# Kernel tuning notes

Hardware: AMD Instinct MI355X
Metric: run time of the kernel (lower is better)

Reference implementation:

```python
import jax, jax.numpy as jnp
import numpy as np

B, T, C = 16, 512, 768
MULT = 4
D_IN = C * MULT          # 3072
HIDDEN = 1024
N_DATES = 16
STACK_SIZE, STACK_STRIDE = 4, 2
MAX_F = 512
N_MASK_TYPES = 5
N_SESSIONS = 4
SCALE = HIDDEN ** 0.5


def setup_inputs() -> dict:
    key = jax.random.key(0)
    ks = jax.random.split(key, 12)
    inp = {
        "spikes": jax.random.normal(ks[0], (B, T, C), dtype=jnp.float32),
        "spikes_mask": jnp.ones((B, T), dtype=jnp.int64),
        "spikes_timestamp": jax.random.randint(ks[1], (B, T), 0, 255).astype(jnp.int64),
        "date_idx": jax.random.randint(ks[2], (B,), 0, N_DATES).astype(jnp.int64),
        "mask_idx": 1,
        "session_idx": 3,
        # params
        "W_embed": jax.random.normal(ks[3], (N_DATES, D_IN, C), dtype=jnp.float32) * 0.02,
        "b_embed": jax.random.normal(ks[4], (N_DATES, D_IN), dtype=jnp.float32) * 0.02,
        "W_stack": jax.random.normal(ks[5], (HIDDEN, D_IN * STACK_SIZE), dtype=jnp.float32) * 0.02,
        "b_stack": jax.random.normal(ks[6], (HIDDEN,), dtype=jnp.float32) * 0.02,
        "pos_table": jax.random.normal(ks[7], (MAX_F, HIDDEN), dtype=jnp.float32) * 0.02,
        "prompt_table": jax.random.normal(ks[8], (N_MASK_TYPES, HIDDEN), dtype=jnp.float32) * 0.02,
        "session_table": jax.random.normal(ks[9], (N_SESSIONS, HIDDEN), dtype=jnp.float32) * 0.02,
    }
    return inp


def reference(spikes, spikes_mask, spikes_timestamp, date_idx, mask_idx, session_idx,
              W_embed, b_embed, W_stack, b_stack, pos_table, prompt_table, session_table):
    Bb = spikes.shape[0]
    # adapt branch: per-sample expert Linear, done as one gather + batched GEMM
    W = W_embed[date_idx]                      # [B, D_IN, C]
    b = b_embed[date_idx]                      # [B, D_IN]
    x = jnp.einsum('btc,bdc->btd', spikes, W) + b[:, None, :]   # [B, T, D_IN]
    x = jax.nn.gelu(x, approximate=False) * SCALE
    # unfold-based stacking: sliding windows over time
    L = (T - STACK_SIZE) // STACK_STRIDE + 1   # 255
    starts = jnp.arange(L) * STACK_STRIDE
    widx = starts[:, None] + jnp.arange(STACK_SIZE)             # [L, size]
    win = x[:, widx, :]                                         # [B, L, size, D_IN]
    stacked = win.reshape(Bb, L, STACK_SIZE * D_IN)
    x = stacked @ W_stack.T + b_stack                           # [B, L, HIDDEN]
    ts = spikes_timestamp[:, :L]
    mask = jnp.prod(spikes_mask[:, widx], axis=-1)              # [B, L]
    # positional embedding
    x = x + pos_table[ts]
    # prompt token
    x = jnp.concatenate(
        [jnp.broadcast_to(prompt_table[mask_idx][None, None, :], (Bb, 1, HIDDEN)), x], axis=1)
    mask = jnp.pad(mask, ((0, 0), (1, 0)), constant_values=1)
    ts = jnp.concatenate([jnp.zeros((Bb, 1), ts.dtype), ts + 1], axis=1)
    # session token
    x = jnp.concatenate(
        [jnp.broadcast_to(session_table[session_idx][None, None, :], (Bb, 1, HIDDEN)), x], axis=1)
    mask = jnp.pad(mask, ((0, 0), (1, 0)), constant_values=1)
    ts = jnp.concatenate([jnp.zeros((Bb, 1), ts.dtype), ts + 1], axis=1)
    # dropout is identity in eval
    return x, mask, ts
```

## Files before the change

### kernel.cpp

```cpp
#include <hip/hip_runtime.h>
#include <hip/hip_bf16.h>

#define BATCH   16
#define TT      512
#define CC      768
#define D_IN    3072
#define HIDDEN  1024
#define LL      255
#define OUTROWS 257
#define KSTACK  12288
#define N_DATES 16

typedef float f32x4 __attribute__((ext_vector_type(4)));
typedef __bf16 bf16x8 __attribute__((ext_vector_type(8)));
typedef unsigned short u16;

__device__ __forceinline__ u16 f2bf(float f) {
    unsigned u = __builtin_bit_cast(unsigned, f);
    u = (u + 0x7FFFu + ((u >> 16) & 1u)) >> 16;
    return (u16)u;
}

__device__ __forceinline__ bf16x8 lds_read8(const u16* p) {
    return __builtin_bit_cast(bf16x8, *(const uint4*)p);
}

__device__ __forceinline__ void gload16(const u16* g, u16* l) {
    __builtin_amdgcn_global_load_lds(
        (const __attribute__((address_space(1))) void*)g,
        (__attribute__((address_space(3))) void*)l, 16, 0, 0);
}

__global__ __launch_bounds__(256) void cvt_wstack(const float* __restrict__ W, u16* __restrict__ out) {
    size_t i = ((size_t)blockIdx.x * 256 + threadIdx.x) * 4;
    size_t stride = (size_t)gridDim.x * 256 * 4;
    for (; i < (size_t)HIDDEN * KSTACK; i += stride) {
        float4 v = *(const float4*)(W + i);
        ushort4 o = make_ushort4(f2bf(v.x), f2bf(v.y), f2bf(v.z), f2bf(v.w));
        *(ushort4*)(out + i) = o;
    }
}

__global__ __launch_bounds__(256) void cvt_spikes(const float* __restrict__ in, u16* __restrict__ out) {
    size_t i = ((size_t)blockIdx.x * 256 + threadIdx.x) * 4;
    size_t stride = (size_t)gridDim.x * 256 * 4;
    for (; i < (size_t)BATCH * TT * CC; i += stride) {
        float4 v = *(const float4*)(in + i);
        ushort4 o = make_ushort4(f2bf(v.x), f2bf(v.y), f2bf(v.z), f2bf(v.w));
        *(ushort4*)(out + i) = o;
    }
}

__global__ __launch_bounds__(64) void date_flags(const int* __restrict__ date_idx, int* __restrict__ flags) {
    const int tid = threadIdx.x;
    if (tid < N_DATES) flags[tid] = 0;
    __syncthreads();
    if (tid < BATCH) flags[date_idx[tid]] = 1;
}

__global__ __launch_bounds__(256) void cvt_wembed(const float* __restrict__ W,
                                                  const int* __restrict__ flags,
                                                  u16* __restrict__ out) {
    const int date = blockIdx.y;
    if (!flags[date]) return;
    const size_t bofs = (size_t)date * D_IN * CC;
    const size_t i = bofs + ((size_t)blockIdx.x * 256 + threadIdx.x) * 4;
    float4 v = *(const float4*)(W + i);
    ushort4 o = make_ushort4(f2bf(v.x), f2bf(v.y), f2bf(v.z), f2bf(v.w));
    *(ushort4*)(out + i) = o;
}

__global__ __launch_bounds__(256, 2) void gemm1_bf(const u16* __restrict__ spk,
                                                   const u16* __restrict__ wemb,
                                                   const float* __restrict__ b_embed,
                                                   const int* __restrict__ date_idx,
                                                   u16* __restrict__ x1) {
    const int nwg = 512;
    const int cpx = nwg / 8;
    const int f   = blockIdx.x;
    const int swz = (f & 7) * cpx + (f >> 3);
    const int bb  = swz >> 5;
    const int rem = swz & 31;
    const int m0  = (rem >> 4) * 256;
    const int n0  = (rem & 15) * 192;

    const int date = date_idx[bb];
    const u16* A  = spk  + (size_t)bb   * TT * CC;
    const u16* Bw = wemb + (size_t)date * D_IN * CC;
    const int S = CC / 32;

    __shared__ u16 Asm[2][128 * 64];
    __shared__ u16 Bsm[2][96 * 64];

    const int tid  = threadIdx.x;
    const int lane = tid & 63;
    const int wave = tid >> 6;
    const int wm = wave >> 1;
    const int wn = wave & 1;

    const int lrow  = lane >> 3;
    const int scol  = ((lane & 7) ^ lrow) << 3;
    const int chalf = scol >> 5;
    const int gk    = scol & 31;

    f32x4 acc[8][6] = {};

    auto STAGE = [&](int slice, int slot) {
        const int k0 = slice * 32;
        u16* Ad = Asm[slot];
        u16* Bd = Bsm[slot];
        #pragma unroll
        for (int i = 0; i < 4; ++i) {
            const int rbase = wave * 32 + i * 8;
            const int tr = 2 * (rbase + lrow) + chalf;
            gload16(A + (size_t)(m0 + tr) * CC + k0 + gk, Ad + rbase * 64);
        }
        #pragma unroll
        for (int i = 0; i < 3; ++i) {
            const int rbase = wave * 24 + i * 8;
            const int tr = 2 * (rbase + lrow) + chalf;
            gload16(Bw + (size_t)(n0 + tr) * CC + k0 + gk, Bd + rbase * 64);
        }
    };

    const int krow  = lane & 15;
    const int kcol  = (lane >> 4) << 3;
    const int cfrag = (kcol + ((krow & 1) << 5)) ^ ((krow >> 1) << 3);
    const int urow  = krow >> 1;

    STAGE(0, 0); STAGE(1, 1);
    for (int t = 0; t < S; ++t) {
        if (t + 1 < S) { asm volatile("s_waitcnt vmcnt(7)" ::: "memory"); }
        else           { asm volatile("s_waitcnt vmcnt(0)" ::: "memory"); }
        __builtin_amdgcn_s_barrier();
        const u16* Ab = Asm[t & 1];
        const u16* Bb = Bsm[t & 1];
        bf16x8 bfr[6];
        #pragma unroll
        for (int j = 0; j < 6; ++j)
            bfr[j] = lds_read8(&Bb[(wn * 48 + j * 8 + urow) * 64 + cfrag]);
        __builtin_amdgcn_s_setprio(1);
        #pragma unroll
        for (int i = 0; i < 8; ++i) {
            bf16x8 af = lds_read8(&Ab[(wm * 64 + i * 8 + urow) * 64 + cfrag]);
            #pragma unroll
            for (int j = 0; j < 6; ++j)
                acc[i][j] = __builtin_amdgcn_mfma_f32_16x16x32_bf16(af, bfr[j], acc[i][j], 0, 0, 0);
        }
        __builtin_amdgcn_s_setprio(0);
        __builtin_amdgcn_s_barrier();
        if (t + 2 < S) STAGE(t + 2, t & 1);
    }

    const float* be = b_embed + (size_t)date * D_IN;
    #pragma unroll
    for (int i = 0; i < 8; ++i) {
        #pragma unroll
        for (int j = 0; j < 6; ++j) {
            const int col  = n0 + wn * 96 + j * 16 + (lane & 15);
            const float bias = be[col];
            const int rbase = m0 + wm * 128 + i * 16 + ((lane >> 4) << 2);
            #pragma unroll
            for (int q = 0; q < 4; ++q) {
                float v = acc[i][j][q] + bias;
                float g = 0.5f * v * (1.0f + erff(v * 0.70710678118654752f)) * 32.0f;
                x1[(size_t)bb * TT * D_IN + (size_t)(rbase + q) * D_IN + col] = f2bf(g);
            }
        }
    }
}

__global__ __launch_bounds__(256) void gemm1_f32(const float* __restrict__ spikes,
                                                 const float* __restrict__ W_embed,
                                                 const float* __restrict__ b_embed,
                                                 const int* __restrict__ date_idx,
                                                 u16* __restrict__ x1) {
    const int m0 = blockIdx.x * 128;
    const int n0 = blockIdx.y * 128;
    const int bb = blockIdx.z;
    const int date = date_idx[bb];
    const float* A  = spikes  + (size_t)bb  * TT * CC;
    const float* Bw = W_embed + (size_t)date * D_IN * CC;

    __shared__ u16 As[128 * 64];
    __shared__ u16 Bs[128 * 64];

    const int tid  = threadIdx.x;
    const int lane = tid & 63;
    const int wave = tid >> 6;
    const int wm = wave >> 1, wn = wave & 1;

    f32x4 acc[4][4] = {};

    for (int k0 = 0; k0 < CC; k0 += 64) {
        {
            const int c4 = tid & 15;
            int r = tid >> 4;
            #pragma unroll
            for (int p = 0; p < 8; ++p, r += 16) {
                float4 va = *(const float4*)(A  + (size_t)(m0 + r) * CC + k0 + c4 * 4);
                float4 vb = *(const float4*)(Bw + (size_t)(n0 + r) * CC + k0 + c4 * 4);
                const int col = c4 * 4;
                const int idx = r * 64 + (col ^ ((r & 7) << 3));
                *(ushort4*)(&As[idx]) = make_ushort4(f2bf(va.x), f2bf(va.y), f2bf(va.z), f2bf(va.w));
                *(ushort4*)(&Bs[idx]) = make_ushort4(f2bf(vb.x), f2bf(vb.y), f2bf(vb.z), f2bf(vb.w));
            }
        }
        __syncthreads();
        #pragma unroll
        for (int kk = 0; kk < 64; kk += 32) {
            bf16x8 af[4], bfr[4];
            const int krow = lane & 15;
            const int kcol = kk + ((lane >> 4) << 3);
            #pragma unroll
            for (int i = 0; i < 4; ++i) {
                const int ra = wm * 64 + i * 16 + krow;
                af[i]  = lds_read8(&As[ra * 64 + (kcol ^ ((ra & 7) << 3))]);
                const int rb = wn * 64 + i * 16 + krow;
                bfr[i] = lds_read8(&Bs[rb * 64 + (kcol ^ ((rb & 7) << 3))]);
            }
            #pragma unroll
            for (int i = 0; i < 4; ++i)
                #pragma unroll
                for (int j = 0; j < 4; ++j)
                    acc[i][j] = __builtin_amdgcn_mfma_f32_16x16x32_bf16(af[i], bfr[j], acc[i][j], 0, 0, 0);
        }
        __syncthreads();
    }

    const float* be = b_embed + (size_t)date * D_IN;
    #pragma unroll
    for (int i = 0; i < 4; ++i) {
        #pragma unroll
        for (int j = 0; j < 4; ++j) {
            const int col  = n0 + wn * 64 + j * 16 + (lane & 15);
            const float bias = be[col];
            const int rbase = m0 + wm * 64 + i * 16 + ((lane >> 4) << 2);
            #pragma unroll
            for (int q = 0; q < 4; ++q) {
                float v = acc[i][j][q] + bias;
                float g = 0.5f * v * (1.0f + erff(v * 0.70710678118654752f)) * 32.0f;
                x1[(size_t)bb * TT * D_IN + (size_t)(rbase + q) * D_IN + col] = f2bf(g);
            }
        }
    }
}

template <bool WRITE_PART>
__global__ __launch_bounds__(256, 4) void gemm2(const u16* __restrict__ x1,
                                                const u16* __restrict__ Wbf,
                                                float* __restrict__ part,
                                                const float* __restrict__ b_stack,
                                                const float* __restrict__ pos_table,
                                                const int* __restrict__ tstamp,
                                                float* __restrict__ out,
                                                int KS) {
    const int nwg = 8 * KS * BATCH;
    const int cpx = nwg / 8;
    const int f   = blockIdx.x;
    const int swz = (f & 7) * cpx + (f >> 3);
    const int bb  = swz / (8 * KS);
    const int rem = swz % (8 * KS);
    const int ks  = rem / 8;
    const int n0  = (rem % 8) * 128;

    const int KCH  = KSTACK / KS;
    const int kbeg = ks * KCH;
    const int S    = KCH / 32;
    const u16* Xb = x1 + (size_t)bb * TT * D_IN;

    __shared__ u16 Asm[3][128 * 64];
    __shared__ u16 Bsm[3][64 * 64];

    const int tid  = threadIdx.x;
    const int lane = tid & 63;
    const int wave = tid >> 6;
    const int wm = wave >> 1;
    const int wn = wave & 1;

    const int lrow  = lane >> 3;
    const int scol  = ((lane & 7) ^ lrow) << 3;
    const int chalf = scol >> 5;
    const int gk    = scol & 31;

    f32x4 acc[8][4] = {};

    auto STAGE = [&](int slice, int slot) {
        const int k0 = kbeg + slice * 32;
        const int s  = k0 / D_IN;
        const int d0 = k0 % D_IN;
        u16* Ad = Asm[slot];
        u16* Bd = Bsm[slot];
        #pragma unroll
        for (int p = 0; p < 4; ++p) {
            const int rbase = (wave + 4 * p) * 8;
            const int tr = 2 * (rbase + lrow) + chalf;
            gload16(Xb + (size_t)(2 * tr + s) * D_IN + d0 + gk, Ad + rbase * 64);
        }
        #pragma unroll
        for (int p = 0; p < 2; ++p) {
            const int rbase = (wave + 4 * p) * 8;
            const int tr = 2 * (rbase + lrow) + chalf;
            gload16(Wbf + (size_t)(n0 + tr) * KSTACK + k0 + gk, Bd + rbase * 64);
        }
    };

    const int krow  = lane & 15;
    const int kcol  = (lane >> 4) << 3;
    const int cfrag = (kcol + ((krow & 1) << 5)) ^ ((krow >> 1) << 3);
    const int urow  = krow >> 1;

    STAGE(0, 0); STAGE(1, 1);
    int cur = 0;
    for (int t = 0; t < S; ++t) {
        if (t + 1 < S) { asm volatile("s_waitcnt vmcnt(6)" ::: "memory"); }
        else           { asm volatile("s_waitcnt vmcnt(0)" ::: "memory"); }
        __builtin_amdgcn_s_barrier();
        const u16* Ab = Asm[cur];
        const u16* Bb = Bsm[cur];
        bf16x8 af[8], bfr[4];
        #pragma unroll
        for (int i = 0; i < 8; ++i)
            af[i] = lds_read8(&Ab[(wm * 64 + i * 8 + urow) * 64 + cfrag]);
        #pragma unroll
        for (int j = 0; j < 4; ++j)
            bfr[j] = lds_read8(&Bb[(wn * 32 + j * 8 + urow) * 64 + cfrag]);
        if (t + 2 < S) {
            const int slot2 = (cur + 2 >= 3) ? cur - 1 : cur + 2;
            STAGE(t + 2, slot2);
        }
        __builtin_amdgcn_s_setprio(1);
        #pragma unroll
        for (int i = 0; i < 8; ++i)
            #pragma unroll
            for (int j = 0; j < 4; ++j)
                acc[i][j] = __builtin_amdgcn_mfma_f32_16x16x32_bf16(af[i], bfr[j], acc[i][j], 0, 0, 0);
        __builtin_amdgcn_s_setprio(0);
        cur = (cur + 1 >= 3) ? 0 : cur + 1;
    }

    if (WRITE_PART) {
        float* pt = part + ((size_t)(ks * BATCH + bb) * 256) * HIDDEN;
        #pragma unroll
        for (int i = 0; i < 8; ++i) {
            #pragma unroll
            for (int j = 0; j < 4; ++j) {
                const int col = n0 + wn * 64 + j * 16 + (lane & 15);
                const int rb  = wm * 128 + i * 16 + ((lane >> 4) << 2);
                #pragma unroll
                for (int q = 0; q < 4; ++q)
                    pt[(size_t)(rb + q) * HIDDEN + col] = acc[i][j][q];
            }
        }
    } else {
        #pragma unroll
        for (int i = 0; i < 8; ++i) {
            #pragma unroll
            for (int j = 0; j < 4; ++j) {
                const int col = n0 + wn * 64 + j * 16 + (lane & 15);
                const int lb  = wm * 128 + i * 16 + ((lane >> 4) << 2);
                #pragma unroll
                for (int q = 0; q < 4; ++q) {
                    const int l = lb + q;
                    if (l < LL) {
                        const int tsv = tstamp[bb * TT + l];
                        float v = acc[i][j][q] + b_stack[col] + pos_table[(size_t)tsv * HIDDEN + col];
                        out[(size_t)bb * OUTROWS * HIDDEN + (size_t)(2 + l) * HIDDEN + col] = v;
                    }
                }
            }
        }
    }
}

__global__ __launch_bounds__(256) void reduce_ep(const float* __restrict__ part,
                                                 const float* __restrict__ b_stack,
                                                 const float* __restrict__ pos_table,
                                                 const int* __restrict__ tstamp,
                                                 float* __restrict__ out,
                                                 int KS) {
    const int idx = blockIdx.x * 256 + threadIdx.x;
    const int c4  = idx & (HIDDEN / 4 - 1);
    const int r   = idx >> 8;
    if (r >= BATCH * LL) return;
    const int l  = r % LL;
    const int bb = r / LL;
    float4 v = make_float4(0.f, 0.f, 0.f, 0.f);
    for (int ks = 0; ks < KS; ++ks) {
        float4 p = *(const float4*)(part + ((size_t)(ks * BATCH + bb) * 256 + l) * HIDDEN + c4 * 4);
        v.x += p.x; v.y += p.y; v.z += p.z; v.w += p.w;
    }
    const int tsv = tstamp[bb * TT + l];
    float4 bs = *(const float4*)(b_stack + c4 * 4);
    float4 ps = *(const float4*)(pos_table + (size_t)tsv * HIDDEN + c4 * 4);
    v.x += bs.x + ps.x; v.y += bs.y + ps.y; v.z += bs.z + ps.z; v.w += bs.w + ps.w;
    *(float4*)(out + ((size_t)bb * OUTROWS + 2 + l) * HIDDEN + c4 * 4) = v;
}

__global__ __launch_bounds__(256) void epilogue_misc(const int* __restrict__ smask,
                                                     const int* __restrict__ tstamp,
                                                     const int* __restrict__ mask_idx_p,
                                                     const int* __restrict__ session_idx_p,
                                                     const float* __restrict__ prompt_table,
                                                     const float* __restrict__ session_table,
                                                     float* __restrict__ out) {
    const int bb = blockIdx.x;
    const int tid = threadIdx.x;
    const int mi = mask_idx_p[0];
    const int si = session_idx_p[0];
    float* xb = out + (size_t)bb * OUTROWS * HIDDEN;
    for (int i = tid; i < HIDDEN; i += 256) {
        xb[i]          = session_table[(size_t)si * HIDDEN + i];
        xb[HIDDEN + i] = prompt_table[(size_t)mi * HIDDEN + i];
    }
    float* maskout = out + (size_t)BATCH * OUTROWS * HIDDEN + (size_t)bb * OUTROWS;
    float* tsout   = out + (size_t)BATCH * OUTROWS * HIDDEN + (size_t)BATCH * OUTROWS + (size_t)bb * OUTROWS;
    for (int j = tid; j < OUTROWS; j += 256) {
        if (j == 0)      { maskout[0] = 1.0f; tsout[0] = 0.0f; }
        else if (j == 1) { maskout[1] = 1.0f; tsout[1] = 1.0f; }
        else {
            const int l = j - 2;
            int m = 1;
            #pragma unroll
            for (int s = 0; s < 4; ++s) m *= smask[bb * TT + 2 * l + s];
            maskout[j] = (float)m;
            tsout[j]   = (float)(tstamp[bb * TT + l] + 2);
        }
    }
}

extern "C" void kernel_launch(void* const* d_in, const int* in_sizes, int n_in,
                              void* d_out, int out_size, void* d_ws, size_t ws_size,
                              hipStream_t stream) {
    const float* spikes      = (const float*)d_in[0];
    const int*   spikes_mask = (const int*)d_in[1];
    const int*   tstamp      = (const int*)d_in[2];
    const int*   date_idx    = (const int*)d_in[3];
    const int*   mask_idx    = (const int*)d_in[4];
    const int*   session_idx = (const int*)d_in[5];
    const float* W_embed     = (const float*)d_in[6];
    const float* b_embed     = (const float*)d_in[7];
    const float* W_stack     = (const float*)d_in[8];
    const float* b_stack     = (const float*)d_in[9];
    const float* pos_table   = (const float*)d_in[10];
    const float* prompt_tab  = (const float*)d_in[11];
    const float* session_tab = (const float*)d_in[12];
    float* out = (float*)d_out;

    const size_t X1_B   = (size_t)BATCH * TT * D_IN * 2;
    const size_t WBF_B  = (size_t)HIDDEN * KSTACK * 2;
    const size_t PART_B = (size_t)BATCH * 256 * HIDDEN * 4;
    const size_t FLAGS_B = 4096;
    const size_t SPK_B  = (size_t)BATCH * TT * CC * 2;
    const size_t WEMB_B = (size_t)N_DATES * D_IN * CC * 2;
    const size_t BASE   = X1_B + WBF_B;
    const size_t UNION_BF = FLAGS_B + SPK_B + WEMB_B;

    u16*   x1    = (u16*)d_ws;
    u16*   Wbf   = (u16*)((char*)d_ws + X1_B);
    int*   flags = (int*)((char*)d_ws + BASE);
    u16*   spkbf = (u16*)((char*)d_ws + BASE + FLAGS_B);
    u16*   wembf = (u16*)((char*)d_ws + BASE + FLAGS_B + SPK_B);
    float* part  = (float*)((char*)d_ws + BASE);

    const bool use_bf = (ws_size >= BASE + UNION_BF);
    int KS = 0;
    if (use_bf) KS = 4;
    else {
        size_t rem = (ws_size > BASE) ? (ws_size - BASE) : 0;
        KS = (int)(rem / PART_B); if (KS > 4) KS = 4;
    }

    cvt_wstack<<<2048, 256, 0, stream>>>(W_stack, Wbf);

    if (use_bf) {
        date_flags<<<1, 64, 0, stream>>>(date_idx, flags);
        cvt_spikes<<<2048, 256, 0, stream>>>(spikes, spkbf);
        cvt_wembed<<<dim3(D_IN * CC / 4 / 256, N_DATES), 256, 0, stream>>>(W_embed, flags, wembf);
        gemm1_bf<<<512, 256, 0, stream>>>(spkbf, wembf, b_embed, date_idx, x1);
    } else {
        gemm1_f32<<<dim3(TT / 128, D_IN / 128, BATCH), 256, 0, stream>>>(spikes, W_embed, b_embed, date_idx, x1);
    }

    if (KS > 0) {
        gemm2<true><<<8 * KS * BATCH, 256, 0, stream>>>(x1, Wbf, part, b_stack, pos_table, tstamp, out, KS);
        reduce_ep<<<(BATCH * LL * (HIDDEN / 4) + 255) / 256, 256, 0, stream>>>(part, b_stack, pos_table, tstamp, out, KS);
    } else {
        gemm2<false><<<8 * 1 * BATCH, 256, 0, stream>>>(x1, Wbf, part, b_stack, pos_table, tstamp, out, 1);
    }
    epilogue_misc<<<BATCH, 256, 0, stream>>>(spikes_mask, tstamp, mask_idx, session_idx,
                                             prompt_tab, session_tab, out);
}
```

Baseline: 248.0 us.

## Fuse conversion kernels and split gemm2 M tile in half for more workgroups

```diff
diff --git a/kernel.cpp b/kernel.cpp
--- a/kernel.cpp
+++ b/kernel.cpp
@@ -31,43 +31,37 @@
         (__attribute__((address_space(3))) void*)l, 16, 0, 0);
 }
 
-__global__ __launch_bounds__(256) void cvt_wstack(const float* __restrict__ W, u16* __restrict__ out) {
-    size_t i = ((size_t)blockIdx.x * 256 + threadIdx.x) * 4;
-    size_t stride = (size_t)gridDim.x * 256 * 4;
-    for (; i < (size_t)HIDDEN * KSTACK; i += stride) {
-        float4 v = *(const float4*)(W + i);
+__global__ __launch_bounds__(256) void cvt_all(const float* __restrict__ Ws,
+                                               const float* __restrict__ spk,
+                                               const float* __restrict__ We,
+                                               const int* __restrict__ date_idx,
+                                               u16* __restrict__ oWs, u16* __restrict__ oSpk,
+                                               u16* __restrict__ oWe, int do_bf) {
+    __shared__ int dates[BATCH];
+    if (threadIdx.x < BATCH) dates[threadIdx.x] = date_idx[threadIdx.x];
+    __syncthreads();
+    const size_t NW = (size_t)HIDDEN * KSTACK / 4;
+    const size_t NS = (size_t)BATCH * TT * CC / 4;
+    const size_t NE = (size_t)N_DATES * D_IN * CC / 4;
+    const unsigned DSZ = (unsigned)(D_IN * CC / 4);
+    const size_t total = do_bf ? (NW + NS + NE) : NW;
+    for (size_t i = (size_t)blockIdx.x * 256 + threadIdx.x; i < total; i += (size_t)gridDim.x * 256) {
+        const float* src; u16* dst; size_t off;
+        if (i < NW)            { src = Ws;  dst = oWs;  off = i; }
+        else if (i < NW + NS)  { src = spk; dst = oSpk; off = i - NW; }
+        else {
+            off = i - NW - NS;
+            const int date = (int)((unsigned)off / DSZ);
+            bool used = false;
+            #pragma unroll
+            for (int b = 0; b < BATCH; ++b) used |= (dates[b] == date);
+            if (!used) continue;
+            src = We; dst = oWe;
+        }
+        float4 v = *(const float4*)(src + off * 4);
         ushort4 o = make_ushort4(f2bf(v.x), f2bf(v.y), f2bf(v.z), f2bf(v.w));
-        *(ushort4*)(out + i) = o;
-    }
-}
-
-__global__ __launch_bounds__(256) void cvt_spikes(const float* __restrict__ in, u16* __restrict__ out) {
-    size_t i = ((size_t)blockIdx.x * 256 + threadIdx.x) * 4;
-    size_t stride = (size_t)gridDim.x * 256 * 4;
-    for (; i < (size_t)BATCH * TT * CC; i += stride) {
-        float4 v = *(const float4*)(in + i);
-        ushort4 o = make_ushort4(f2bf(v.x), f2bf(v.y), f2bf(v.z), f2bf(v.w));
-        *(ushort4*)(out + i) = o;
-    }
-}
-
-__global__ __launch_bounds__(64) void date_flags(const int* __restrict__ date_idx, int* __restrict__ flags) {
-    const int tid = threadIdx.x;
-    if (tid < N_DATES) flags[tid] = 0;
-    __syncthreads();
-    if (tid < BATCH) flags[date_idx[tid]] = 1;
-}
-
-__global__ __launch_bounds__(256) void cvt_wembed(const float* __restrict__ W,
-                                                  const int* __restrict__ flags,
-                                                  u16* __restrict__ out) {
-    const int date = blockIdx.y;
-    if (!flags[date]) return;
-    const size_t bofs = (size_t)date * D_IN * CC;
-    const size_t i = bofs + ((size_t)blockIdx.x * 256 + threadIdx.x) * 4;
-    float4 v = *(const float4*)(W + i);
-    ushort4 o = make_ushort4(f2bf(v.x), f2bf(v.y), f2bf(v.z), f2bf(v.w));
-    *(ushort4*)(out + i) = o;
+        *(ushort4*)(dst + off * 4) = o;
+    }
 }
 
 __global__ __launch_bounds__(256, 2) void gemm1_bf(const u16* __restrict__ spk,
@@ -255,22 +249,25 @@
                                                 const int* __restrict__ tstamp,
                                                 float* __restrict__ out,
                                                 int KS) {
-    const int nwg = 8 * KS * BATCH;
+    const int nwg = 2 * 8 * KS * BATCH;
     const int cpx = nwg / 8;
     const int f   = blockIdx.x;
     const int swz = (f & 7) * cpx + (f >> 3);
-    const int bb  = swz / (8 * KS);
-    const int rem = swz % (8 * KS);
-    const int ks  = rem / 8;
-    const int n0  = (rem % 8) * 128;
+    const int perb = 2 * 8 * KS;
+    const int bb  = swz / perb;
+    int r = swz % perb;
+    const int ks  = r / 16;
+    r &= 15;
+    const int n0  = (r >> 1) * 128;
+    const int mq  = r & 1;
 
     const int KCH  = KSTACK / KS;
     const int kbeg = ks * KCH;
     const int S    = KCH / 32;
     const u16* Xb = x1 + (size_t)bb * TT * D_IN;
 
-    __shared__ u16 Asm[3][128 * 64];
-    __shared__ u16 Bsm[3][64 * 64];
+    __shared__ u16 Asm[2][64 * 64];
+    __shared__ u16 Bsm[2][64 * 64];
 
     const int tid  = threadIdx.x;
     const int lane = tid & 63;
@@ -283,7 +280,7 @@
     const int chalf = scol >> 5;
     const int gk    = scol & 31;
 
-    f32x4 acc[8][4] = {};
+    f32x4 acc[4][4] = {};
 
     auto STAGE = [&](int slice, int slot) {
         const int k0 = kbeg + slice * 32;
@@ -292,10 +289,10 @@
         u16* Ad = Asm[slot];
         u16* Bd = Bsm[slot];
         #pragma unroll
-        for (int p = 0; p < 4; ++p) {
+        for (int p = 0; p < 2; ++p) {
             const int rbase = (wave + 4 * p) * 8;
             const int tr = 2 * (rbase + lrow) + chalf;
-            gload16(Xb + (size_t)(2 * tr + s) * D_IN + d0 + gk, Ad + rbase * 64);
+            gload16(Xb + (size_t)(2 * (mq * 128 + tr) + s) * D_IN + d0 + gk, Ad + rbase * 64);
         }
         #pragma unroll
         for (int p = 0; p < 2; ++p) {
@@ -311,42 +308,38 @@
     const int urow  = krow >> 1;
 
     STAGE(0, 0); STAGE(1, 1);
-    int cur = 0;
     for (int t = 0; t < S; ++t) {
-        if (t + 1 < S) { asm volatile("s_waitcnt vmcnt(6)" ::: "memory"); }
+        if (t + 1 < S) { asm volatile("s_waitcnt vmcnt(4)" ::: "memory"); }
         else           { asm volatile("s_waitcnt vmcnt(0)" ::: "memory"); }
         __builtin_amdgcn_s_barrier();
-        const u16* Ab = Asm[cur];
-        const u16* Bb = Bsm[cur];
-        bf16x8 af[8], bfr[4];
-        #pragma unroll
-        for (int i = 0; i < 8; ++i)
-            af[i] = lds_read8(&Ab[(wm * 64 + i * 8 + urow) * 64 + cfrag]);
+        const u16* Ab = Asm[t & 1];
+        const u16* Bb = Bsm[t & 1];
+        bf16x8 af[4], bfr[4];
+        #pragma unroll
+        for (int i = 0; i < 4; ++i)
+            af[i] = lds_read8(&Ab[(wm * 32 + i * 8 + urow) * 64 + cfrag]);
         #pragma unroll
         for (int j = 0; j < 4; ++j)
             bfr[j] = lds_read8(&Bb[(wn * 32 + j * 8 + urow) * 64 + cfrag]);
-        if (t + 2 < S) {
-            const int slot2 = (cur + 2 >= 3) ? cur - 1 : cur + 2;
-            STAGE(t + 2, slot2);
-        }
         __builtin_amdgcn_s_setprio(1);
         #pragma unroll
-        for (int i = 0; i < 8; ++i)
+        for (int i = 0; i < 4; ++i)
             #pragma unroll
             for (int j = 0; j < 4; ++j)
                 acc[i][j] = __builtin_amdgcn_mfma_f32_16x16x32_bf16(af[i], bfr[j], acc[i][j], 0, 0, 0);
         __builtin_amdgcn_s_setprio(0);
-        cur = (cur + 1 >= 3) ? 0 : cur + 1;
+        __builtin_amdgcn_s_barrier();
+        if (t + 2 < S) STAGE(t + 2, t & 1);
     }
 
     if (WRITE_PART) {
         float* pt = part + ((size_t)(ks * BATCH + bb) * 256) * HIDDEN;
         #pragma unroll
-        for (int i = 0; i < 8; ++i) {
+        for (int i = 0; i < 4; ++i) {
             #pragma unroll
             for (int j = 0; j < 4; ++j) {
                 const int col = n0 + wn * 64 + j * 16 + (lane & 15);
-                const int rb  = wm * 128 + i * 16 + ((lane >> 4) << 2);
+                const int rb  = mq * 128 + wm * 64 + i * 16 + ((lane >> 4) << 2);
                 #pragma unroll
                 for (int q = 0; q < 4; ++q)
                     pt[(size_t)(rb + q) * HIDDEN + col] = acc[i][j][q];
@@ -354,11 +347,11 @@
         }
     } else {
         #pragma unroll
-        for (int i = 0; i < 8; ++i) {
+        for (int i = 0; i < 4; ++i) {
             #pragma unroll
             for (int j = 0; j < 4; ++j) {
                 const int col = n0 + wn * 64 + j * 16 + (lane & 15);
-                const int lb  = wm * 128 + i * 16 + ((lane >> 4) << 2);
+                const int lb  = mq * 128 + wm * 64 + i * 16 + ((lane >> 4) << 2);
                 #pragma unroll
                 for (int q = 0; q < 4; ++q) {
                     const int l = lb + q;
@@ -450,17 +443,15 @@
     const size_t X1_B   = (size_t)BATCH * TT * D_IN * 2;
     const size_t WBF_B  = (size_t)HIDDEN * KSTACK * 2;
     const size_t PART_B = (size_t)BATCH * 256 * HIDDEN * 4;
-    const size_t FLAGS_B = 4096;
     const size_t SPK_B  = (size_t)BATCH * TT * CC * 2;
     const size_t WEMB_B = (size_t)N_DATES * D_IN * CC * 2;
     const size_t BASE   = X1_B + WBF_B;
-    const size_t UNION_BF = FLAGS_B + SPK_B + WEMB_B;
+    const size_t UNION_BF = SPK_B + WEMB_B;
 
     u16*   x1    = (u16*)d_ws;
     u16*   Wbf   = (u16*)((char*)d_ws + X1_B);
-    int*   flags = (int*)((char*)d_ws + BASE);
-    u16*   spkbf = (u16*)((char*)d_ws + BASE + FLAGS_B);
-    u16*   wembf = (u16*)((char*)d_ws + BASE + FLAGS_B + SPK_B);
+    u16*   spkbf = (u16*)((char*)d_ws + BASE);
+    u16*   wembf = (u16*)((char*)d_ws + BASE + SPK_B);
     float* part  = (float*)((char*)d_ws + BASE);
 
     const bool use_bf = (ws_size >= BASE + UNION_BF);
@@ -471,22 +462,20 @@
         KS = (int)(rem / PART_B); if (KS > 4) KS = 4;
     }
 
-    cvt_wstack<<<2048, 256, 0, stream>>>(W_stack, Wbf);
+    cvt_all<<<2048, 256, 0, stream>>>(W_stack, spikes, W_embed, date_idx,
+                                      Wbf, spkbf, wembf, use_bf ? 1 : 0);
 
     if (use_bf) {
-        date_flags<<<1, 64, 0, stream>>>(date_idx, flags);
-        cvt_spikes<<<2048, 256, 0, stream>>>(spikes, spkbf);
-        cvt_wembed<<<dim3(D_IN * CC / 4 / 256, N_DATES), 256, 0, stream>>>(W_embed, flags, wembf);
         gemm1_bf<<<512, 256, 0, stream>>>(spkbf, wembf, b_embed, date_idx, x1);
     } else {
         gemm1_f32<<<dim3(TT / 128, D_IN / 128, BATCH), 256, 0, stream>>>(spikes, W_embed, b_embed, date_idx, x1);
     }
 
     if (KS > 0) {
-        gemm2<true><<<8 * KS * BATCH, 256, 0, stream>>>(x1, Wbf, part, b_stack, pos_table, tstamp, out, KS);
+        gemm2<true><<<2 * 8 * KS * BATCH, 256, 0, stream>>>(x1, Wbf, part, b_stack, pos_table, tstamp, out, KS);
         reduce_ep<<<(BATCH * LL * (HIDDEN / 4) + 255) / 256, 256, 0, stream>>>(part, b_stack, pos_table, tstamp, out, KS);
     } else {
-        gemm2<false><<<8 * 1 * BATCH, 256, 0, stream>>>(x1, Wbf, part, b_stack, pos_table, tstamp, out, 1);
+        gemm2<false><<<2 * 8 * 1 * BATCH, 256, 0, stream>>>(x1, Wbf, part, b_stack, pos_table, tstamp, out, 1);
     }
     epilogue_misc<<<BATCH, 256, 0, stream>>>(spikes_mask, tstamp, mask_idx, session_idx,
                                              prompt_tab, session_tab, out);
```

Result: slower. 268.9 us (+8.4%).
